# Optimization experiments

Measured on AMD Instinct MI355X. Metric: run time of the kernel, lower is better.

Reference implementation:

```python
import jax, jax.numpy as jnp
import numpy as np

N, E, NF, EF = 2048, 65536, 128, 64
HID, NH, HD, FF, L = 256, 8, 32, 1024, 4
OUT, MAXN = 1280, 4096


def setup_inputs() -> dict:
    key = jax.random.key(0)
    ks = iter(jax.random.split(key, 64))
    def rn(shape, s=0.02):
        return jax.random.normal(next(ks), shape, jnp.float32) * s
    inp = dict(
        node_features=jax.random.normal(next(ks), (N, NF), jnp.float32),
        edge_features=jax.random.normal(next(ks), (E, EF), jnp.float32),
        edge_index=jax.random.randint(next(ks), (2, E), 0, N),
        W_node=rn((NF, HID)), b_node=jnp.zeros((HID,)),
        W_edge=rn((EF, HID)), b_edge=jnp.zeros((HID,)),
        pos_emb=rn((MAXN, HID), 1.0),
        Wq=rn((L, HID, HID)), bq=jnp.zeros((L, HID)),
        Wk=rn((L, HID, HID)), bk=jnp.zeros((L, HID)),
        Wv=rn((L, HID, HID)), bv=jnp.zeros((L, HID)),
        Wo=rn((L, HID, HID)), bo=jnp.zeros((L, HID)),
        Wep=rn((L, HID, NH)), bep=jnp.zeros((L, NH)),
        Wf1=rn((L, HID, FF)), bf1=jnp.zeros((L, FF)),
        Wf2=rn((L, FF, HID)), bf2=jnp.zeros((L, HID)),
        g1=jnp.ones((L, HID)), be1=jnp.zeros((L, HID)),
        g2=jnp.ones((L, HID)), be2=jnp.zeros((L, HID)),
        g_ln=jnp.ones((HID,)), b_ln=jnp.zeros((HID,)),
        Wp1=rn((HID, HID)), bp1=jnp.zeros((HID,)),
        Wp2=rn((HID, 1)), bp2=jnp.zeros((1,)),
        Wo1=rn((3 * HID, 2 * HID)), bo1=jnp.zeros((2 * HID,)),
        Wo2=rn((2 * HID, OUT)), bo2=jnp.zeros((OUT,)),
    )
    return inp


def _ln(x, g, b, eps=1e-5):
    m = x.mean(-1, keepdims=True)
    v = ((x - m) ** 2).mean(-1, keepdims=True)
    return (x - m) * jax.lax.rsqrt(v + eps) * g + b


def reference(node_features, edge_features, edge_index, W_node, b_node, W_edge,
              b_edge, pos_emb, Wq, bq, Wk, bk, Wv, bv, Wo, bo, Wep, bep,
              Wf1, bf1, Wf2, bf2, g1, be1, g2, be2, g_ln, b_ln,
              Wp1, bp1, Wp2, bp2, Wo1, bo1, Wo2, bo2):
    n = node_features.shape[0]
    src, dst = edge_index[0], edge_index[1]
    scale = float(np.sqrt(HD))
    # node encoding + learned positional embedding (n <= max_nodes path)
    x = node_features @ W_node + b_node + pos_emb[:n]
    edge_attr = edge_features @ W_edge + b_edge  # [E, HID]
    # symmetric adjacency mask with self-loops
    adj = jnp.zeros((n, n), bool).at[src, dst].set(True).at[dst, src].set(True)
    adj = adj.at[jnp.arange(n), jnp.arange(n)].set(True)
    for i in range(L):
        Q = (x @ Wq[i] + bq[i]).reshape(n, NH, HD)
        K = (x @ Wk[i] + bk[i]).reshape(n, NH, HD)
        V = (x @ Wv[i] + bv[i]).reshape(n, NH, HD)
        scores = jnp.einsum('nhd,mhd->nmh', Q, K) / scale  # [n, n, NH]
        ebias = edge_attr @ Wep[i] + bep[i]  # [E, NH]
        scores = scores.at[src, dst].add(ebias)  # accumulating scatter, same as per-edge loop
        scores = jnp.where(adj[:, None, :], scores.transpose(0, 2, 1), -jnp.inf)  # [n, NH, n]
        attn = jax.nn.softmax(scores, axis=-1)
        ctx = jnp.einsum('nhm,mhd->nhd', attn, V).reshape(n, HID)
        a = ctx @ Wo[i] + bo[i]
        x = _ln(x + a, g1[i], be1[i])
        f = jax.nn.gelu(x @ Wf1[i] + bf1[i], approximate=False) @ Wf2[i] + bf2[i]
        x = _ln(x + f, g2[i], be2[i])
    x = _ln(x, g_ln, b_ln)
    # global pooling (batch=None path): mean / max / attention
    mean_p = x.mean(0, keepdims=True)
    max_p = x.max(0, keepdims=True)
    aw = jax.nn.softmax(jnp.tanh(x @ Wp1 + bp1) @ Wp2 + bp2, axis=0)  # [n, 1]
    attn_p = (x * aw).sum(0, keepdims=True)
    g = jnp.concatenate([mean_p, max_p, attn_p], axis=1)  # [1, 3*HID]
    out = jax.nn.relu(g @ Wo1 + bo1) @ Wo2 + bo2  # [1, OUT]
    return out
```

## Files before the change

kernel.cpp:

```cpp
#include <hip/hip_runtime.h>
#include <math.h>

#define NNODE 2048
#define NEDGE 65536
#define HIDN  256
#define NHEAD 8
#define HDIM  32
#define FFD   1024
#define NLAYER 4
#define OUTD  1280
#define NNZ_MAX (2*NEDGE + NNODE)

typedef __attribute__((ext_vector_type(8))) short bf16x8;
typedef __attribute__((ext_vector_type(4))) float f32x4;

__device__ __forceinline__ unsigned short f2b(float f) {
    unsigned u = __float_as_uint(f);
    unsigned r = (u + 0x7fffu + ((u >> 16) & 1u)) >> 16;
    return (unsigned short)r;
}
__device__ __forceinline__ float b2f(unsigned short u) {
    return __uint_as_float((unsigned)u << 16);
}

template<int K, int EPI, int OUT>
__global__ __launch_bounds__(256)
void mgemm(const unsigned short* __restrict__ A, const unsigned short* __restrict__ Bt,
           const float* __restrict__ bias, const float* __restrict__ extra,
           float* __restrict__ Cf, unsigned short* __restrict__ Cb,
           int M, int N, const float* __restrict__ Wp2, float* __restrict__ sred)
{
    __shared__ __align__(16) unsigned short As[64 * 40];
    __shared__ __align__(16) unsigned short Bs[64 * 40];
    int tid = threadIdx.x;
    int bm0 = blockIdx.y * 64, bn0 = blockIdx.x * 64;
    int wave = tid >> 6, lane = tid & 63;
    int wm = (wave >> 1) * 32, wn = (wave & 1) * 32;
    int srow = tid >> 2, skoff = (tid & 3) * 8;
    int lrow = lane & 15, quad = lane >> 4;
    const unsigned short* ap = A  + (size_t)(bm0 + srow) * K + skoff;
    const unsigned short* bp = Bt + (size_t)(bn0 + srow) * K + skoff;
    uint4 av = *(const uint4*)ap;
    uint4 bv = *(const uint4*)bp;
    f32x4 acc[2][2] = {};
    constexpr int NC = K / 32;
    #pragma unroll 8
    for (int c = 0; c < NC; ++c) {
        *(uint4*)(&As[srow*40 + skoff]) = av;
        *(uint4*)(&Bs[srow*40 + skoff]) = bv;
        __syncthreads();
        if (c + 1 < NC) {
            av = *(const uint4*)(ap + (c+1)*32);
            bv = *(const uint4*)(bp + (c+1)*32);
        }
        bf16x8 af[2], bfr[2];
        #pragma unroll
        for (int i = 0; i < 2; i++) af[i]  = *(const bf16x8*)(&As[(wm + i*16 + lrow)*40 + quad*8]);
        #pragma unroll
        for (int j = 0; j < 2; j++) bfr[j] = *(const bf16x8*)(&Bs[(wn + j*16 + lrow)*40 + quad*8]);
        #pragma unroll
        for (int i = 0; i < 2; i++)
            #pragma unroll
            for (int j = 0; j < 2; j++)
                acc[i][j] = __builtin_amdgcn_mfma_f32_16x16x32_bf16(af[i], bfr[j], acc[i][j], 0, 0, 0);
        __syncthreads();
    }
    if (EPI == 4) {
        #pragma unroll
        for (int i = 0; i < 2; i++) {
            #pragma unroll
            for (int r = 0; r < 4; r++) {
                int row = bm0 + wm + i*16 + quad*4 + r;
                float ps = 0.f;
                #pragma unroll
                for (int j = 0; j < 2; j++) {
                    int col = bn0 + wn + j*16 + lrow;
                    float v = tanhf(acc[i][j][r] + bias[col]);
                    ps += v * Wp2[col];
                }
                ps += __shfl_xor(ps, 1);
                ps += __shfl_xor(ps, 2);
                ps += __shfl_xor(ps, 4);
                ps += __shfl_xor(ps, 8);
                if (lrow == 0) atomicAdd(&sred[row], ps);
            }
        }
        return;
    }
    #pragma unroll
    for (int i = 0; i < 2; i++)
        #pragma unroll
        for (int j = 0; j < 2; j++) {
            int col = bn0 + wn + j*16 + lrow;
            float bvv = bias[col];
            #pragma unroll
            for (int r = 0; r < 4; r++) {
                int row = bm0 + wm + i*16 + quad*4 + r;
                float v = acc[i][j][r] + bvv;
                if (EPI == 1) v = 0.5f * v * (1.f + erff(v * 0.70710678118654752f));
                else if (EPI == 2) v = tanhf(v);
                else if (EPI == 3) v += extra[(size_t)row*N + col];
                if (OUT == 0 || OUT == 2) Cf[(size_t)row*N + col] = v;
                if (OUT == 1 || OUT == 2) Cb[(size_t)row*N + col] = f2b(v);
            }
        }
}

__global__ __launch_bounds__(256)
void transpose_all(const float* __restrict__ Wq, const float* __restrict__ Wk,
                   const float* __restrict__ Wv, const float* __restrict__ Wo,
                   const float* __restrict__ Wf1, const float* __restrict__ Wf2,
                   const float* __restrict__ W_node, const float* __restrict__ Wp1,
                   unsigned short* __restrict__ WqkvT, unsigned short* __restrict__ WoT,
                   unsigned short* __restrict__ Wf1T, unsigned short* __restrict__ Wf2T,
                   unsigned short* __restrict__ WnT, unsigned short* __restrict__ Wp1T)
{
    __shared__ unsigned short tile[32][33];
    int bid = blockIdx.x;
    const float* s; unsigned short* d; int K, N, n0, k0;
    if (bid < 1024) {
        int mat = bid >> 6, rem = bid & 63;
        int m4 = mat & 3, l = mat >> 2;
        s = (m4 == 0 ? Wq : m4 == 1 ? Wk : m4 == 2 ? Wv : Wo) + (size_t)l * 65536;
        d = (m4 < 3) ? WqkvT + (size_t)l*196608 + (size_t)m4*65536
                     : WoT + (size_t)l*65536;
        K = 256; N = 256; n0 = (rem & 7) * 32; k0 = (rem >> 3) * 32;
    } else if (bid < 2048) {
        int idx = bid - 1024; int l = idx >> 8, rem = idx & 255;
        s = Wf1 + (size_t)l*262144; d = Wf1T + (size_t)l*262144;
        K = 256; N = 1024; n0 = (rem & 31) * 32; k0 = (rem >> 5) * 32;
    } else if (bid < 3072) {
        int idx = bid - 2048; int l = idx >> 8, rem = idx & 255;
        s = Wf2 + (size_t)l*262144; d = Wf2T + (size_t)l*262144;
        K = 1024; N = 256; n0 = (rem & 7) * 32; k0 = (rem >> 3) * 32;
    } else if (bid < 3104) {
        int rem = bid - 3072;
        s = W_node; d = WnT;
        K = 128; N = 256; n0 = (rem & 7) * 32; k0 = (rem >> 3) * 32;
    } else {
        int rem = bid - 3104;
        s = Wp1; d = Wp1T;
        K = 256; N = 256; n0 = (rem & 7) * 32; k0 = (rem >> 3) * 32;
    }
    int tx = threadIdx.x & 31, ty = threadIdx.x >> 5;
    #pragma unroll
    for (int i = 0; i < 4; i++)
        tile[ty + i*8][tx] = f2b(s[(size_t)(k0 + ty + i*8) * N + n0 + tx]);
    __syncthreads();
    #pragma unroll
    for (int i = 0; i < 4; i++)
        d[(size_t)(n0 + ty + i*8) * K + k0 + tx] = tile[tx][ty + i*8];
}

__global__ void misc_prep(const float* __restrict__ nf, unsigned short* __restrict__ nf_b,
                          const float* __restrict__ bq, const float* __restrict__ bk,
                          const float* __restrict__ bv, float* __restrict__ bqkv)
{
    int t = blockIdx.x * 256 + threadIdx.x;
    if (t < NNODE*128) {
        nf_b[t] = f2b(nf[t]);
    } else {
        int u = t - NNODE*128;
        if (u < NLAYER*768) {
            int l = u / 768, j = u % 768;
            float v = (j < 256) ? bq[l*256 + j] : (j < 512 ? bk[l*256 + j - 256] : bv[l*256 + j - 512]);
            bqkv[u] = v;
        }
    }
}

__global__ void adj_build(const int* __restrict__ src, const int* __restrict__ dst,
                          unsigned* __restrict__ adjbits)
{
    int t = blockIdx.x * blockDim.x + threadIdx.x;
    if (t < NEDGE) {
        int s = src[t], d = dst[t];
        atomicOr(&adjbits[(size_t)s*64 + (d >> 5)], 1u << (d & 31));
        atomicOr(&adjbits[(size_t)d*64 + (s >> 5)], 1u << (s & 31));
    }
    if (t < NNODE)
        atomicOr(&adjbits[(size_t)t*64 + (t >> 5)], 1u << (t & 31));
}

__global__ void row_rank(const unsigned* __restrict__ adjbits,
                         unsigned* __restrict__ rowcum, int* __restrict__ deg)
{
    int i = blockIdx.x * blockDim.x + threadIdx.x;
    if (i >= NNODE) return;
    unsigned c = 0;
    for (int w = 0; w < 64; w++) {
        rowcum[i*64 + w] = c;
        c += __popc(adjbits[i*64 + w]);
    }
    deg[i] = (int)c;
}

__global__ __launch_bounds__(256)
void scan_kernel(const int* __restrict__ deg, int* __restrict__ rowoff)
{
    __shared__ int part[256];
    int tid = threadIdx.x;
// ... 113 lines not shown
            float p  = __expf(s - mn);
            ushort4 vu = *(const ushort4*)(QKVb + (size_t)j*768 + 512 + off);
            acc.x = acc.x*sc + p*b2f(vu.x);
            acc.y = acc.y*sc + p*b2f(vu.y);
            acc.z = acc.z*sc + p*b2f(vu.z);
            acc.w = acc.w*sc + p*b2f(vu.w);
            l = l*sc + p;
            m = mn;
        }
    }
    if ((lane & 7) == 0) { mS[w][h] = m; lS[w][h] = l; }
    *(float4*)&accS[w][off] = acc;
    __syncthreads();
    if (w == 0) {
        float m0 = mS[0][h], m1 = mS[1][h], m2 = mS[2][h], m3 = mS[3][h];
        float mx = fmaxf(fmaxf(m0, m1), fmaxf(m2, m3));
        float e0 = (m0 == -INFINITY) ? 0.f : __expf(m0 - mx);
        float e1 = (m1 == -INFINITY) ? 0.f : __expf(m1 - mx);
        float e2 = (m2 == -INFINITY) ? 0.f : __expf(m2 - mx);
        float e3 = (m3 == -INFINITY) ? 0.f : __expf(m3 - mx);
        float ls = lS[0][h]*e0 + lS[1][h]*e1 + lS[2][h]*e2 + lS[3][h]*e3;
        float4 a0 = *(float4*)&accS[0][off];
        float4 a1 = *(float4*)&accS[1][off];
        float4 a2 = *(float4*)&accS[2][off];
        float4 a3 = *(float4*)&accS[3][off];
        float inv = 1.f / ls;
        ushort4 o;
        o.x = f2b((a0.x*e0 + a1.x*e1 + a2.x*e2 + a3.x*e3) * inv);
        o.y = f2b((a0.y*e0 + a1.y*e1 + a2.y*e2 + a3.y*e3) * inv);
        o.z = f2b((a0.z*e0 + a1.z*e1 + a2.z*e2 + a3.z*e3) * inv);
        o.w = f2b((a0.w*e0 + a1.w*e1 + a2.w*e2 + a3.w*e3) * inv);
        *(ushort4*)(ctxb + (size_t)i*HIDN + off) = o;
    }
}

template<bool RES>
__global__ __launch_bounds__(256)
void ln_kernel(float* __restrict__ x, const float* __restrict__ r,
               const float* __restrict__ g, const float* __restrict__ b,
               unsigned short* __restrict__ xb)
{
    __shared__ float lds[4];
    int row = blockIdx.x, c = threadIdx.x;
    float v = x[(size_t)row*HIDN + c];
    if (RES) v += r[(size_t)row*HIDN + c];
    float s = v;
    for (int mm = 1; mm < 64; mm <<= 1) s += __shfl_xor(s, mm);
    if ((c & 63) == 0) lds[c >> 6] = s;
    __syncthreads();
    float mean = (lds[0] + lds[1] + lds[2] + lds[3]) * (1.f / HIDN);
    __syncthreads();
    float dv = v - mean;
    float qq = dv * dv;
    for (int mm = 1; mm < 64; mm <<= 1) qq += __shfl_xor(qq, mm);
    if ((c & 63) == 0) lds[c >> 6] = qq;
    __syncthreads();
    float var = (lds[0] + lds[1] + lds[2] + lds[3]) * (1.f / HIDN);
    float rs = rsqrtf(var + 1e-5f);
    float o = dv * rs * g[c] + b[c];
    x[(size_t)row*HIDN + c] = o;
    xb[(size_t)row*HIDN + c] = f2b(o);
}

__global__ __launch_bounds__(256)
void pool_part(const float* __restrict__ x, const float* __restrict__ sred,
               float* __restrict__ partial)
{
    __shared__ float red[4];
    __shared__ float aw[128];
    int b = blockIdx.x, tid = threadIdx.x;
    float mxs = -INFINITY;
    for (int r = tid; r < NNODE; r += 256) mxs = fmaxf(mxs, sred[r]);
    for (int mm = 1; mm < 64; mm <<= 1) mxs = fmaxf(mxs, __shfl_xor(mxs, mm));
    if ((tid & 63) == 0) red[tid >> 6] = mxs;
    __syncthreads();
    mxs = fmaxf(fmaxf(red[0], red[1]), fmaxf(red[2], red[3]));
    __syncthreads();
    float ss = 0.f;
    for (int r = tid; r < NNODE; r += 256) ss += __expf(sred[r] - mxs);
    for (int mm = 1; mm < 64; mm <<= 1) ss += __shfl_xor(ss, mm);
    if ((tid & 63) == 0) red[tid >> 6] = ss;
    __syncthreads();
    ss = red[0] + red[1] + red[2] + red[3];
    float inv = 1.f / ss;
    int r0 = b * 128;
    if (tid < 128) aw[tid] = __expf(sred[r0 + tid] - mxs) * inv;
    __syncthreads();
    float sm = 0.f, mx = -INFINITY, ap = 0.f;
    for (int r = 0; r < 128; r++) {
        float v = x[(size_t)(r0 + r)*HIDN + tid];
        sm += v;
        mx = fmaxf(mx, v);
        ap += v * aw[r];
    }
// ... 75 lines not shown
    const float* bv = (const float*)d_in[13];
    const float* Wo = (const float*)d_in[14];
    const float* bo = (const float*)d_in[15];
    const float* Wep = (const float*)d_in[16];
    const float* bep = (const float*)d_in[17];
    const float* Wf1 = (const float*)d_in[18];
    const float* bf1 = (const float*)d_in[19];
    const float* Wf2 = (const float*)d_in[20];
    const float* bf2 = (const float*)d_in[21];
    const float* g1  = (const float*)d_in[22];
    const float* be1 = (const float*)d_in[23];
    const float* g2  = (const float*)d_in[24];
    const float* be2 = (const float*)d_in[25];
    const float* g_ln = (const float*)d_in[26];
    const float* b_ln = (const float*)d_in[27];
    const float* Wp1 = (const float*)d_in[28];
    const float* bp1 = (const float*)d_in[29];
    const float* Wp2 = (const float*)d_in[30];
    const float* bp2 = (const float*)d_in[31];
    const float* Wo1 = (const float*)d_in[32];
    const float* bo1 = (const float*)d_in[33];
    const float* Wo2 = (const float*)d_in[34];
    const float* bo2 = (const float*)d_in[35];
    (void)bp2;
    const int* src = edge_index;
    const int* dst = edge_index + NEDGE;

    char* w = (char*)d_ws;
    auto carve = [&](size_t nbytes) {
        void* p = (void*)w;
        w += (nbytes + 255) & ~(size_t)255;
        return p;
    };
    float* x        = (float*)carve((size_t)NNODE*HIDN*4);
    unsigned short* xb = (unsigned short*)carve((size_t)NNODE*HIDN*2);
    unsigned short* bufQKVb = (unsigned short*)carve((size_t)NNODE*768*2);
    float* bufO     = (float*)carve((size_t)NNODE*HIDN*4);
    unsigned short* bufAb = (unsigned short*)carve((size_t)NNODE*HIDN*2);
    unsigned short* bufFb = (unsigned short*)carve((size_t)NNODE*FFD*2);
    float* Wcomb    = (float*)carve(64*32*4);
    float* bcomb    = (float*)carve(32*4);
    unsigned* adjbits = (unsigned*)carve((size_t)NNODE*64*4);
    float* bias_csr = (float*)carve((size_t)NNZ_MAX*32*4);
    float* sbuf  = (float*)carve(NNODE*4);
    unsigned* rowcum  = (unsigned*)carve((size_t)NNODE*64*4);
    int* deg    = (int*)carve(NNODE*4);
    int* rowoff = (int*)carve((NNODE+1)*4);
    int* colsb  = (int*)carve((size_t)NNZ_MAX*4);
    float* gbuf  = (float*)carve(3*HIDN*4);
    float* partial = (float*)carve(16*768*4);
    float* h1buf = (float*)carve(512*4);
    unsigned short* nf_b  = (unsigned short*)carve((size_t)NNODE*128*2);
    unsigned short* WnT   = (unsigned short*)carve((size_t)HIDN*128*2);
    unsigned short* WqkvT = (unsigned short*)carve((size_t)NLAYER*768*HIDN*2);
    float*          bqkv  = (float*)carve((size_t)NLAYER*768*4);
    unsigned short* WoT   = (unsigned short*)carve((size_t)NLAYER*HIDN*HIDN*2);
    unsigned short* Wf1T  = (unsigned short*)carve((size_t)NLAYER*FFD*HIDN*2);
    unsigned short* Wf2T  = (unsigned short*)carve((size_t)NLAYER*HIDN*FFD*2);
    unsigned short* Wp1T  = (unsigned short*)carve((size_t)HIDN*HIDN*2);

    hipMemsetAsync(adjbits, 0,
                   (size_t)NNODE*64*4 + (size_t)NNZ_MAX*32*4 + (size_t)NNODE*4, stream);
    adj_build<<<(NEDGE+255)/256, 256, 0, stream>>>(src, dst, adjbits);
    row_rank<<<NNODE/256, 256, 0, stream>>>(adjbits, rowcum, deg);
    scan_kernel<<<1, 256, 0, stream>>>(deg, rowoff);
    fill_cols<<<(NNODE*64)/256, 256, 0, stream>>>(adjbits, rowoff, rowcum, colsb);
    wcomb_kernel<<<(64*32+32+255)/256, 256, 0, stream>>>(W_edge, b_edge, Wep, bep, Wcomb, bcomb);
    edge_bias_scatter<<<(NEDGE*32)/256, 256, 0, stream>>>(
        edge_features, Wcomb, bcomb, src, dst, adjbits, rowcum, rowoff, bias_csr);

    misc_prep<<<(NNODE*128 + NLAYER*768 + 255)/256, 256, 0, stream>>>(
        node_features, nf_b, bq, bk, bv, bqkv);
    transpose_all<<<3168, 256, 0, stream>>>(Wq, Wk, Wv, Wo, Wf1, Wf2, W_node, Wp1,
                                            WqkvT, WoT, Wf1T, Wf2T, WnT, Wp1T);

    mgemm<128,3,2><<<dim3(HIDN/64, NNODE/64), 256, 0, stream>>>(
        nf_b, WnT, b_node, pos_emb, x, xb, NNODE, HIDN, nullptr, nullptr);

    for (int l = 0; l < NLAYER; l++) {
        mgemm<256,0,1><<<dim3(768/64, NNODE/64), 256, 0, stream>>>(
            xb, WqkvT + (size_t)l*768*HIDN, bqkv + l*768, nullptr, nullptr, bufQKVb, NNODE, 768, nullptr, nullptr);
        attn_kernel<<<NNODE, 256, 0, stream>>>(bufQKVb, rowoff, colsb, bias_csr, bufAb, l);
        mgemm<256,0,0><<<dim3(HIDN/64, NNODE/64), 256, 0, stream>>>(
            bufAb, WoT + (size_t)l*HIDN*HIDN, bo + l*HIDN, nullptr, bufO, nullptr, NNODE, HIDN, nullptr, nullptr);
        ln_kernel<true><<<NNODE, 256, 0, stream>>>(x, bufO, g1 + l*HIDN, be1 + l*HIDN, xb);
        mgemm<256,1,1><<<dim3(FFD/64, NNODE/64), 256, 0, stream>>>(
            xb, Wf1T + (size_t)l*FFD*HIDN, bf1 + l*FFD, nullptr, nullptr, bufFb, NNODE, FFD, nullptr, nullptr);
        mgemm<1024,0,0><<<dim3(HIDN/64, NNODE/64), 256, 0, stream>>>(
            bufFb, Wf2T + (size_t)l*HIDN*FFD, bf2 + l*HIDN, nullptr, bufO, nullptr, NNODE, HIDN, nullptr, nullptr);
        ln_kernel<true><<<NNODE, 256, 0, stream>>>(x, bufO, g2 + l*HIDN, be2 + l*HIDN, xb);
    }

    ln_kernel<false><<<NNODE, 256, 0, stream>>>(x, nullptr, g_ln, b_ln, xb);
    mgemm<256,4,0><<<dim3(HIDN/64, NNODE/64), 256, 0, stream>>>(
        xb, Wp1T, bp1, nullptr, nullptr, nullptr, NNODE, HIDN, Wp2, sbuf);
    pool_part<<<16, 256, 0, stream>>>(x, sbuf, partial);
    pool_fin<<<1, 256, 0, stream>>>(partial, gbuf);
    head1<<<8, 256, 0, stream>>>(gbuf, Wo1, bo1, h1buf);
    head2<<<OUTD/64, 256, 0, stream>>>(h1buf, Wo2, bo2, (float*)d_out);
}
```

Baseline: 462.4 us.

## Fuse output and FFN2 GEMMs with residual LayerNorm; merge prep kernels

```diff
diff --git a/kernel.cpp b/kernel.cpp
--- a/kernel.cpp
+++ b/kernel.cpp
@@ -98,12 +98,154 @@
                 int row = bm0 + wm + i*16 + quad*4 + r;
                 float v = acc[i][j][r] + bvv;
                 if (EPI == 1) v = 0.5f * v * (1.f + erff(v * 0.70710678118654752f));
-                else if (EPI == 2) v = tanhf(v);
                 else if (EPI == 3) v += extra[(size_t)row*N + col];
                 if (OUT == 0 || OUT == 2) Cf[(size_t)row*N + col] = v;
                 if (OUT == 1 || OUT == 2) Cb[(size_t)row*N + col] = f2b(v);
             }
         }
+}
+
+template<int K, bool DOUBLE>
+__global__ __launch_bounds__(256)
+void mgemm_ln(const unsigned short* __restrict__ A, const unsigned short* __restrict__ Bt,
+              const float* __restrict__ bias, const float* __restrict__ res,
+              const float* __restrict__ ga, const float* __restrict__ ba,
+              const float* __restrict__ gb, const float* __restrict__ bb,
+              float* __restrict__ X, unsigned short* __restrict__ Xb)
+{
+    __shared__ __align__(16) unsigned short As[16 * 40];
+    __shared__ __align__(16) unsigned short Bs[256 * 40];
+    __shared__ float rsum[4][16], rsq[4][16], rsum2[4][16], rsq2[4][16];
+    int tid = threadIdx.x;
+    int bm0 = blockIdx.x * 16;
+    int w = tid >> 6, lane = tid & 63;
+    int lrow = lane & 15, quad = lane >> 4;
+    int arow = tid >> 2, akoff = (tid & 3) * 8;
+    const unsigned short* ap = A + (size_t)(bm0 + arow) * K + akoff;
+    const unsigned short* bp = Bt + (size_t)tid * K;
+    uint4 av, bv0, bv1, bv2, bv3;
+    if (tid < 64) av = *(const uint4*)ap;
+    bv0 = *(const uint4*)(bp + 0);
+    bv1 = *(const uint4*)(bp + 8);
+    bv2 = *(const uint4*)(bp + 16);
+    bv3 = *(const uint4*)(bp + 24);
+    f32x4 acc[4] = {};
+    constexpr int NC = K / 32;
+    #pragma unroll 8
+    for (int c = 0; c < NC; ++c) {
+        if (tid < 64) *(uint4*)(&As[arow*40 + akoff]) = av;
+        *(uint4*)(&Bs[tid*40 + 0])  = bv0;
+        *(uint4*)(&Bs[tid*40 + 8])  = bv1;
+        *(uint4*)(&Bs[tid*40 + 16]) = bv2;
+        *(uint4*)(&Bs[tid*40 + 24]) = bv3;
+        __syncthreads();
+        if (c + 1 < NC) {
+            if (tid < 64) av = *(const uint4*)(ap + (c+1)*32);
+            bv0 = *(const uint4*)(bp + (c+1)*32 + 0);
+            bv1 = *(const uint4*)(bp + (c+1)*32 + 8);
+            bv2 = *(const uint4*)(bp + (c+1)*32 + 16);
+            bv3 = *(const uint4*)(bp + (c+1)*32 + 24);
+        }
+        bf16x8 af = *(const bf16x8*)(&As[lrow*40 + quad*8]);
+        #pragma unroll
+        for (int j = 0; j < 4; j++) {
+            bf16x8 bf = *(const bf16x8*)(&Bs[(w*64 + j*16 + lrow)*40 + quad*8]);
+            acc[j] = __builtin_amdgcn_mfma_f32_16x16x32_bf16(af, bf, acc[j], 0, 0, 0);
+        }
+        __syncthreads();
+    }
+    float v[4][4];
+    #pragma unroll
+    for (int j = 0; j < 4; j++) {
+        int col = w*64 + j*16 + lrow;
+        float bvv = bias[col];
+        #pragma unroll
+        for (int r = 0; r < 4; r++) {
+            int row = bm0 + quad*4 + r;
+            v[j][r] = acc[j][r] + bvv + res[(size_t)row*HIDN + col];
+        }
+    }
+    float mean[4], rsv[4];
+    #pragma unroll
+    for (int r = 0; r < 4; r++) {
+        float s = v[0][r] + v[1][r] + v[2][r] + v[3][r];
+        s += __shfl_xor(s, 1); s += __shfl_xor(s, 2);
+        s += __shfl_xor(s, 4); s += __shfl_xor(s, 8);
+        if (lrow == 0) rsum[w][quad*4 + r] = s;
+    }
+    __syncthreads();
+    #pragma unroll
+    for (int r = 0; r < 4; r++) {
+        int rr = quad*4 + r;
+        mean[r] = (rsum[0][rr] + rsum[1][rr] + rsum[2][rr] + rsum[3][rr]) * (1.f/HIDN);
+        float q = 0.f;
+        #pragma unroll
+        for (int j = 0; j < 4; j++) { float d = v[j][r] - mean[r]; q += d*d; }
+        q += __shfl_xor(q, 1); q += __shfl_xor(q, 2);
+        q += __shfl_xor(q, 4); q += __shfl_xor(q, 8);
+        if (lrow == 0) rsq[w][rr] = q;
+    }
+    __syncthreads();
+    #pragma unroll
+    for (int r = 0; r < 4; r++) {
+        int rr = quad*4 + r;
+        float var = (rsq[0][rr] + rsq[1][rr] + rsq[2][rr] + rsq[3][rr]) * (1.f/HIDN);
+        rsv[r] = rsqrtf(var + 1e-5f);
+    }
+    #pragma unroll
+    for (int j = 0; j < 4; j++) {
+        int col = w*64 + j*16 + lrow;
+        float gv = ga[col], bvv = ba[col];
+        #pragma unroll
+        for (int r = 0; r < 4; r++)
+            v[j][r] = (v[j][r] - mean[r]) * rsv[r] * gv + bvv;
+    }
+    if (DOUBLE) {
+        #pragma unroll
+        for (int r = 0; r < 4; r++) {
+            float s = v[0][r] + v[1][r] + v[2][r] + v[3][r];
+            s += __shfl_xor(s, 1); s += __shfl_xor(s, 2);
+            s += __shfl_xor(s, 4); s += __shfl_xor(s, 8);
+            if (lrow == 0) rsum2[w][quad*4 + r] = s;
+        }
+        __syncthreads();
+        #pragma unroll
+        for (int r = 0; r < 4; r++) {
+            int rr = quad*4 + r;
+            mean[r] = (rsum2[0][rr] + rsum2[1][rr] + rsum2[2][rr] + rsum2[3][rr]) * (1.f/HIDN);
+            float q = 0.f;
+            #pragma unroll
+            for (int j = 0; j < 4; j++) { float d = v[j][r] - mean[r]; q += d*d; }
+            q += __shfl_xor(q, 1); q += __shfl_xor(q, 2);
+            q += __shfl_xor(q, 4); q += __shfl_xor(q, 8);
+            if (lrow == 0) rsq2[w][rr] = q;
+        }
+        __syncthreads();
+        #pragma unroll
+        for (int r = 0; r < 4; r++) {
+            int rr = quad*4 + r;
+            float var = (rsq2[0][rr] + rsq2[1][rr] + rsq2[2][rr] + rsq2[3][rr]) * (1.f/HIDN);
+            rsv[r] = rsqrtf(var + 1e-5f);
+        }
+        #pragma unroll
+        for (int j = 0; j < 4; j++) {
+            int col = w*64 + j*16 + lrow;
+            float gv = gb[col], bvv = bb[col];
+            #pragma unroll
+            for (int r = 0; r < 4; r++)
+                v[j][r] = (v[j][r] - mean[r]) * rsv[r] * gv + bvv;
+        }
+    }
+    #pragma unroll
+    for (int j = 0; j < 4; j++) {
+        int col = w*64 + j*16 + lrow;
+        #pragma unroll
+        for (int r = 0; r < 4; r++) {
+            int row = bm0 + quad*4 + r;
+            X[(size_t)row*HIDN + col] = v[j][r];
+            Xb[(size_t)row*HIDN + col] = f2b(v[j][r]);
+        }
+    }
 }
 
 __global__ __launch_bounds__(256)
@@ -113,10 +255,27 @@
                    const float* __restrict__ W_node, const float* __restrict__ Wp1,
                    unsigned short* __restrict__ WqkvT, unsigned short* __restrict__ WoT,
                    unsigned short* __restrict__ Wf1T, unsigned short* __restrict__ Wf2T,
-                   unsigned short* __restrict__ WnT, unsigned short* __restrict__ Wp1T)
+                   unsigned short* __restrict__ WnT, unsigned short* __restrict__ Wp1T,
+                   const float* __restrict__ nf, unsigned short* __restrict__ nf_b,
+                   const float* __restrict__ bq, const float* __restrict__ bk,
+                   const float* __restrict__ bv, float* __restrict__ bqkv)
 {
     __shared__ unsigned short tile[32][33];
     int bid = blockIdx.x;
+    if (bid >= 3168) {
+        int t = (bid - 3168) * 256 + threadIdx.x;
+        if (t < NNODE*128) {
+            nf_b[t] = f2b(nf[t]);
+        } else {
+            int u = t - NNODE*128;
+            if (u < NLAYER*768) {
+                int l = u / 768, j = u % 768;
+                float vv = (j < 256) ? bq[l*256 + j] : (j < 512 ? bk[l*256 + j - 256] : bv[l*256 + j - 512]);
+                bqkv[u] = vv;
+            }
+        }
+        return;
+    }
     const float* s; unsigned short* d; int K, N, n0, k0;
     if (bid < 1024) {
         int mat = bid >> 6, rem = bid & 63;
@@ -150,23 +309,6 @@
     #pragma unroll
     for (int i = 0; i < 4; i++)
         d[(size_t)(n0 + ty + i*8) * K + k0 + tx] = tile[tx][ty + i*8];
-}
-
-__global__ void misc_prep(const float* __restrict__ nf, unsigned short* __restrict__ nf_b,
-                          const float* __restrict__ bq, const float* __restrict__ bk,
-                          const float* __restrict__ bv, float* __restrict__ bqkv)
-{
-    int t = blockIdx.x * 256 + threadIdx.x;
-    if (t < NNODE*128) {
-        nf_b[t] = f2b(nf[t]);
-    } else {
-        int u = t - NNODE*128;
-        if (u < NLAYER*768) {
-            int l = u / 768, j = u % 768;
-            float v = (j < 256) ? bq[l*256 + j] : (j < 512 ? bk[l*256 + j - 256] : bv[l*256 + j - 512]);
-            bqkv[u] = v;
-        }
-    }
 }
 
 __global__ void adj_build(const int* __restrict__ src, const int* __restrict__ dst,
@@ -346,34 +488,6 @@
         o.w = f2b((a0.w*e0 + a1.w*e1 + a2.w*e2 + a3.w*e3) * inv);
         *(ushort4*)(ctxb + (size_t)i*HIDN + off) = o;
     }
-}
-
-template<bool RES>
-__global__ __launch_bounds__(256)
-void ln_kernel(float* __restrict__ x, const float* __restrict__ r,
-               const float* __restrict__ g, const float* __restrict__ b,
-               unsigned short* __restrict__ xb)
-{
-    __shared__ float lds[4];
-    int row = blockIdx.x, c = threadIdx.x;
-    float v = x[(size_t)row*HIDN + c];
-    if (RES) v += r[(size_t)row*HIDN + c];
-    float s = v;
-    for (int mm = 1; mm < 64; mm <<= 1) s += __shfl_xor(s, mm);
-    if ((c & 63) == 0) lds[c >> 6] = s;
-    __syncthreads();
-    float mean = (lds[0] + lds[1] + lds[2] + lds[3]) * (1.f / HIDN);
-    __syncthreads();
-    float dv = v - mean;
-    float qq = dv * dv;
-    for (int mm = 1; mm < 64; mm <<= 1) qq += __shfl_xor(qq, mm);
-    if ((c & 63) == 0) lds[c >> 6] = qq;
-    __syncthreads();
-    float var = (lds[0] + lds[1] + lds[2] + lds[3]) * (1.f / HIDN);
-    float rs = rsqrtf(var + 1e-5f);
-    float o = dv * rs * g[c] + b[c];
-    x[(size_t)row*HIDN + c] = o;
-    xb[(size_t)row*HIDN + c] = f2b(o);
 }
 
 __global__ __launch_bounds__(256)
@@ -518,7 +632,6 @@
     float* x        = (float*)carve((size_t)NNODE*HIDN*4);
     unsigned short* xb = (unsigned short*)carve((size_t)NNODE*HIDN*2);
     unsigned short* bufQKVb = (unsigned short*)carve((size_t)NNODE*768*2);
-    float* bufO     = (float*)carve((size_t)NNODE*HIDN*4);
     unsigned short* bufAb = (unsigned short*)carve((size_t)NNODE*HIDN*2);
     unsigned short* bufFb = (unsigned short*)carve((size_t)NNODE*FFD*2);
     float* Wcomb    = (float*)carve(64*32*4);
@@ -552,10 +665,10 @@
     edge_bias_scatter<<<(NEDGE*32)/256, 256, 0, stream>>>(
         edge_features, Wcomb, bcomb, src, dst, adjbits, rowcum, rowoff, bias_csr);
 
-    misc_prep<<<(NNODE*128 + NLAYER*768 + 255)/256, 256, 0, stream>>>(
+    transpose_all<<<3168 + 1024 + 12, 256, 0, stream>>>(
+        Wq, Wk, Wv, Wo, Wf1, Wf2, W_node, Wp1,
+        WqkvT, WoT, Wf1T, Wf2T, WnT, Wp1T,
         node_features, nf_b, bq, bk, bv, bqkv);
-    transpose_all<<<3168, 256, 0, stream>>>(Wq, Wk, Wv, Wo, Wf1, Wf2, W_node, Wp1,
-                                            WqkvT, WoT, Wf1T, Wf2T, WnT, Wp1T);
 
     mgemm<128,3,2><<<dim3(HIDN/64, NNODE/64), 256, 0, stream>>>(
         nf_b, WnT, b_node, pos_emb, x, xb, NNODE, HIDN, nullptr, nullptr);
@@ -564,17 +677,21 @@
         mgemm<256,0,1><<<dim3(768/64, NNODE/64), 256, 0, stream>>>(
             xb, WqkvT + (size_t)l*768*HIDN, bqkv + l*768, nullptr, nullptr, bufQKVb, NNODE, 768, nullptr, nullptr);
         attn_kernel<<<NNODE, 256, 0, stream>>>(bufQKVb, rowoff, colsb, bias_csr, bufAb, l);
-        mgemm<256,0,0><<<dim3(HIDN/64, NNODE/64), 256, 0, stream>>>(
-            bufAb, WoT + (size_t)l*HIDN*HIDN, bo + l*HIDN, nullptr, bufO, nullptr, NNODE, HIDN, nullptr, nullptr);
-        ln_kernel<true><<<NNODE, 256, 0, stream>>>(x, bufO, g1 + l*HIDN, be1 + l*HIDN, xb);
+        mgemm_ln<256,false><<<NNODE/16, 256, 0, stream>>>(
+            bufAb, WoT + (size_t)l*HIDN*HIDN, bo + l*HIDN, x,
+            g1 + l*HIDN, be1 + l*HIDN, nullptr, nullptr, x, xb);
         mgemm<256,1,1><<<dim3(FFD/64, NNODE/64), 256, 0, stream>>>(
             xb, Wf1T + (size_t)l*FFD*HIDN, bf1 + l*FFD, nullptr, nullptr, bufFb, NNODE, FFD, nullptr, nullptr);
-        mgemm<1024,0,0><<<dim3(HIDN/64, NNODE/64), 256, 0, stream>>>(
-            bufFb, Wf2T + (size_t)l*HIDN*FFD, bf2 + l*HIDN, nullptr, bufO, nullptr, NNODE, HIDN, nullptr, nullptr);
-        ln_kernel<true><<<NNODE, 256, 0, stream>>>(x, bufO, g2 + l*HIDN, be2 + l*HIDN, xb);
-    }
-
-    ln_kernel<false><<<NNODE, 256, 0, stream>>>(x, nullptr, g_ln, b_ln, xb);
+        if (l < NLAYER - 1)
+            mgemm_ln<1024,false><<<NNODE/16, 256, 0, stream>>>(
+                bufFb, Wf2T + (size_t)l*HIDN*FFD, bf2 + l*HIDN, x,
+                g2 + l*HIDN, be2 + l*HIDN, nullptr, nullptr, x, xb);
+        else
+            mgemm_ln<1024,true><<<NNODE/16, 256, 0, stream>>>(
+                bufFb, Wf2T + (size_t)l*HIDN*FFD, bf2 + l*HIDN, x,
+                g2 + l*HIDN, be2 + l*HIDN, g_ln, b_ln, x, xb);
+    }
+
     mgemm<256,4,0><<<dim3(HIDN/64, NNODE/64), 256, 0, stream>>>(
         xb, Wp1T, bp1, nullptr, nullptr, nullptr, NNODE, HIDN, Wp2, sbuf);
     pool_part<<<16, 256, 0, stream>>>(x, sbuf, partial);
```

Measured after the change: 515.1 us. +11.4%, slower.

## Fuse residual LayerNorm into following GEMM prologue and merge prep kernels

Applied to the files above, without the earlier changes.

```diff
diff --git a/kernel.cpp b/kernel.cpp
--- a/kernel.cpp
+++ b/kernel.cpp
@@ -98,10 +98,152 @@
                 int row = bm0 + wm + i*16 + quad*4 + r;
                 float v = acc[i][j][r] + bvv;
                 if (EPI == 1) v = 0.5f * v * (1.f + erff(v * 0.70710678118654752f));
-                else if (EPI == 2) v = tanhf(v);
                 else if (EPI == 3) v += extra[(size_t)row*N + col];
                 if (OUT == 0 || OUT == 2) Cf[(size_t)row*N + col] = v;
                 if (OUT == 1 || OUT == 2) Cb[(size_t)row*N + col] = f2b(v);
+            }
+        }
+}
+
+template<int EPI, int OUT, bool DBL>
+__global__ __launch_bounds__(256)
+void mgemm_pro(const float* __restrict__ pre, const float* __restrict__ res,
+               const unsigned short* __restrict__ Bt, const float* __restrict__ bias,
+               const float* __restrict__ ga, const float* __restrict__ ba,
+               const float* __restrict__ gb, const float* __restrict__ bb,
+               float* __restrict__ Cf, unsigned short* __restrict__ Cb,
+               float* __restrict__ xout,
+               int M, int N, const float* __restrict__ Wp2, float* __restrict__ sred)
+{
+    __shared__ __align__(16) unsigned short As[64 * 264];
+    __shared__ __align__(16) unsigned short Bs[64 * 40];
+    int tid = threadIdx.x;
+    int bm0 = blockIdx.y * 64, bn0 = blockIdx.x * 64;
+    int wave = tid >> 6, lane = tid & 63;
+    int wm = (wave >> 1) * 32, wn = (wave & 1) * 32;
+    int lrow = lane & 15, quad = lane >> 4;
+    int prow = tid >> 2, pcb = (tid & 3) * 4;
+    const float* pp = pre + (size_t)(bm0 + prow) * HIDN + pcb;
+    const float* rp = res + (size_t)(bm0 + prow) * HIDN + pcb;
+    float4 v[16];
+    float sum = 0.f;
+    #pragma unroll
+    for (int i = 0; i < 16; i++) {
+        float4 a = *(const float4*)(pp + i*16);
+        float4 b = *(const float4*)(rp + i*16);
+        a.x += b.x; a.y += b.y; a.z += b.z; a.w += b.w;
+        v[i] = a;
+        sum += a.x + a.y + a.z + a.w;
+    }
+    sum += __shfl_xor(sum, 1); sum += __shfl_xor(sum, 2);
+    float mean = sum * (1.f/256.f);
+    float sq = 0.f;
+    #pragma unroll
+    for (int i = 0; i < 16; i++) {
+        float dx = v[i].x-mean, dy = v[i].y-mean, dz = v[i].z-mean, dw = v[i].w-mean;
+        sq += dx*dx + dy*dy + dz*dz + dw*dw;
+    }
+    sq += __shfl_xor(sq, 1); sq += __shfl_xor(sq, 2);
+    float rs = rsqrtf(sq * (1.f/256.f) + 1e-5f);
+    #pragma unroll
+    for (int i = 0; i < 16; i++) {
+        float4 g4 = *(const float4*)(ga + pcb + i*16);
+        float4 b4 = *(const float4*)(ba + pcb + i*16);
+        v[i].x = (v[i].x - mean) * rs * g4.x + b4.x;
+        v[i].y = (v[i].y - mean) * rs * g4.y + b4.y;
+        v[i].z = (v[i].z - mean) * rs * g4.z + b4.z;
+        v[i].w = (v[i].w - mean) * rs * g4.w + b4.w;
+    }
+    if (DBL) {
+        sum = 0.f;
+        #pragma unroll
+        for (int i = 0; i < 16; i++) sum += v[i].x + v[i].y + v[i].z + v[i].w;
+        sum += __shfl_xor(sum, 1); sum += __shfl_xor(sum, 2);
+        mean = sum * (1.f/256.f);
+        sq = 0.f;
+        #pragma unroll
+        for (int i = 0; i < 16; i++) {
+            float dx = v[i].x-mean, dy = v[i].y-mean, dz = v[i].z-mean, dw = v[i].w-mean;
+            sq += dx*dx + dy*dy + dz*dz + dw*dw;
+        }
+        sq += __shfl_xor(sq, 1); sq += __shfl_xor(sq, 2);
+        rs = rsqrtf(sq * (1.f/256.f) + 1e-5f);
+        #pragma unroll
+        for (int i = 0; i < 16; i++) {
+            float4 g4 = *(const float4*)(gb + pcb + i*16);
+            float4 b4 = *(const float4*)(bb + pcb + i*16);
+            v[i].x = (v[i].x - mean) * rs * g4.x + b4.x;
+            v[i].y = (v[i].y - mean) * rs * g4.y + b4.y;
+            v[i].z = (v[i].z - mean) * rs * g4.z + b4.z;
+            v[i].w = (v[i].w - mean) * rs * g4.w + b4.w;
+        }
+    }
+    #pragma unroll
+    for (int i = 0; i < 16; i++) {
+        ushort4 us = { f2b(v[i].x), f2b(v[i].y), f2b(v[i].z), f2b(v[i].w) };
+        *(ushort4*)(&As[prow*264 + pcb + i*16]) = us;
+    }
+    if (bn0 == 0) {
+        float* xp = xout + (size_t)(bm0 + prow) * HIDN + pcb;
+        #pragma unroll
+        for (int i = 0; i < 16; i++) *(float4*)(xp + i*16) = v[i];
+    }
+    int srow = tid >> 2, skoff = (tid & 3) * 8;
+    const unsigned short* bp = Bt + (size_t)(bn0 + srow) * HIDN + skoff;
+    uint4 bv = *(const uint4*)bp;
+    f32x4 acc[2][2] = {};
+    #pragma unroll
+    for (int c = 0; c < 8; ++c) {
+        *(uint4*)(&Bs[srow*40 + skoff]) = bv;
+        __syncthreads();
+        if (c + 1 < 8) bv = *(const uint4*)(bp + (c+1)*32);
+        bf16x8 af[2], bfr[2];
+        #pragma unroll
+        for (int i = 0; i < 2; i++) af[i]  = *(const bf16x8*)(&As[(wm + i*16 + lrow)*264 + c*32 + quad*8]);
+        #pragma unroll
+        for (int j = 0; j < 2; j++) bfr[j] = *(const bf16x8*)(&Bs[(wn + j*16 + lrow)*40 + quad*8]);
+        #pragma unroll
+        for (int i = 0; i < 2; i++)
+            #pragma unroll
+            for (int j = 0; j < 2; j++)
+                acc[i][j] = __builtin_amdgcn_mfma_f32_16x16x32_bf16(af[i], bfr[j], acc[i][j], 0, 0, 0);
+        __syncthreads();
+    }
+    if (EPI == 4) {
+        #pragma unroll
+        for (int i = 0; i < 2; i++) {
+            #pragma unroll
+            for (int r = 0; r < 4; r++) {
+                int row = bm0 + wm + i*16 + quad*4 + r;
+                float ps = 0.f;
+                #pragma unroll
+                for (int j = 0; j < 2; j++) {
+                    int col = bn0 + wn + j*16 + lrow;
+                    float vv = tanhf(acc[i][j][r] + bias[col]);
+                    ps += vv * Wp2[col];
+                }
+                ps += __shfl_xor(ps, 1);
+                ps += __shfl_xor(ps, 2);
+                ps += __shfl_xor(ps, 4);
+                ps += __shfl_xor(ps, 8);
+                if (lrow == 0) atomicAdd(&sred[row], ps);
+            }
+        }
+        return;
+    }
+    #pragma unroll
+    for (int i = 0; i < 2; i++)
+        #pragma unroll
+        for (int j = 0; j < 2; j++) {
+            int col = bn0 + wn + j*16 + lrow;
+            float bvv = bias[col];
+            #pragma unroll
+            for (int r = 0; r < 4; r++) {
+                int row = bm0 + wm + i*16 + quad*4 + r;
+                float vv = acc[i][j][r] + bvv;
+                if (EPI == 1) vv = 0.5f * vv * (1.f + erff(vv * 0.70710678118654752f));
+                if (OUT == 0) Cf[(size_t)row*N + col] = vv;
+                else          Cb[(size_t)row*N + col] = f2b(vv);
             }
         }
 }
@@ -113,10 +255,27 @@
                    const float* __restrict__ W_node, const float* __restrict__ Wp1,
                    unsigned short* __restrict__ WqkvT, unsigned short* __restrict__ WoT,
                    unsigned short* __restrict__ Wf1T, unsigned short* __restrict__ Wf2T,
-                   unsigned short* __restrict__ WnT, unsigned short* __restrict__ Wp1T)
+                   unsigned short* __restrict__ WnT, unsigned short* __restrict__ Wp1T,
+                   const float* __restrict__ nf, unsigned short* __restrict__ nf_b,
+                   const float* __restrict__ bq, const float* __restrict__ bk,
+                   const float* __restrict__ bv, float* __restrict__ bqkv)
 {
     __shared__ unsigned short tile[32][33];
     int bid = blockIdx.x;
+    if (bid >= 3168) {
+        int t = (bid - 3168) * 256 + threadIdx.x;
+        if (t < NNODE*128) {
+            nf_b[t] = f2b(nf[t]);
+        } else {
+            int u = t - NNODE*128;
+            if (u < NLAYER*768) {
+                int l = u / 768, j = u % 768;
+                float vv = (j < 256) ? bq[l*256 + j] : (j < 512 ? bk[l*256 + j - 256] : bv[l*256 + j - 512]);
+                bqkv[u] = vv;
+            }
+        }
+        return;
+    }
     const float* s; unsigned short* d; int K, N, n0, k0;
     if (bid < 1024) {
         int mat = bid >> 6, rem = bid & 63;
@@ -150,23 +309,6 @@
     #pragma unroll
     for (int i = 0; i < 4; i++)
         d[(size_t)(n0 + ty + i*8) * K + k0 + tx] = tile[tx][ty + i*8];
-}
-
-__global__ void misc_prep(const float* __restrict__ nf, unsigned short* __restrict__ nf_b,
-                          const float* __restrict__ bq, const float* __restrict__ bk,
-                          const float* __restrict__ bv, float* __restrict__ bqkv)
-{
-    int t = blockIdx.x * 256 + threadIdx.x;
-    if (t < NNODE*128) {
-        nf_b[t] = f2b(nf[t]);
-    } else {
-        int u = t - NNODE*128;
-        if (u < NLAYER*768) {
-            int l = u / 768, j = u % 768;
-            float v = (j < 256) ? bq[l*256 + j] : (j < 512 ? bk[l*256 + j - 256] : bv[l*256 + j - 512]);
-            bqkv[u] = v;
-        }
-    }
 }
 
 __global__ void adj_build(const int* __restrict__ src, const int* __restrict__ dst,
@@ -346,34 +488,6 @@
         o.w = f2b((a0.w*e0 + a1.w*e1 + a2.w*e2 + a3.w*e3) * inv);
         *(ushort4*)(ctxb + (size_t)i*HIDN + off) = o;
     }
-}
-
-template<bool RES>
-__global__ __launch_bounds__(256)
-void ln_kernel(float* __restrict__ x, const float* __restrict__ r,
-               const float* __restrict__ g, const float* __restrict__ b,
-               unsigned short* __restrict__ xb)
-{
-    __shared__ float lds[4];
-    int row = blockIdx.x, c = threadIdx.x;
-    float v = x[(size_t)row*HIDN + c];
-    if (RES) v += r[(size_t)row*HIDN + c];
-    float s = v;
-    for (int mm = 1; mm < 64; mm <<= 1) s += __shfl_xor(s, mm);
-    if ((c & 63) == 0) lds[c >> 6] = s;
-    __syncthreads();
-    float mean = (lds[0] + lds[1] + lds[2] + lds[3]) * (1.f / HIDN);
-    __syncthreads();
-    float dv = v - mean;
-    float qq = dv * dv;
-    for (int mm = 1; mm < 64; mm <<= 1) qq += __shfl_xor(qq, mm);
-    if ((c & 63) == 0) lds[c >> 6] = qq;
-    __syncthreads();
-    float var = (lds[0] + lds[1] + lds[2] + lds[3]) * (1.f / HIDN);
-    float rs = rsqrtf(var + 1e-5f);
-    float o = dv * rs * g[c] + b[c];
-    x[(size_t)row*HIDN + c] = o;
-    xb[(size_t)row*HIDN + c] = f2b(o);
 }
 
 __global__ __launch_bounds__(256)
@@ -515,7 +629,8 @@
         w += (nbytes + 255) & ~(size_t)255;
         return p;
     };
-    float* x        = (float*)carve((size_t)NNODE*HIDN*4);
+    float* xA       = (float*)carve((size_t)NNODE*HIDN*4);
+    float* xB       = (float*)carve((size_t)NNODE*HIDN*4);
     unsigned short* xb = (unsigned short*)carve((size_t)NNODE*HIDN*2);
     unsigned short* bufQKVb = (unsigned short*)carve((size_t)NNODE*768*2);
     float* bufO     = (float*)carve((size_t)NNODE*HIDN*4);
@@ -552,32 +667,45 @@
     edge_bias_scatter<<<(NEDGE*32)/256, 256, 0, stream>>>(
         edge_features, Wcomb, bcomb, src, dst, adjbits, rowcum, rowoff, bias_csr);
 
-    misc_prep<<<(NNODE*128 + NLAYER*768 + 255)/256, 256, 0, stream>>>(
+    transpose_all<<<3168 + 1024 + 12, 256, 0, stream>>>(
+        Wq, Wk, Wv, Wo, Wf1, Wf2, W_node, Wp1,
+        WqkvT, WoT, Wf1T, Wf2T, WnT, Wp1T,
         node_features, nf_b, bq, bk, bv, bqkv);
-    transpose_all<<<3168, 256, 0, stream>>>(Wq, Wk, Wv, Wo, Wf1, Wf2, W_node, Wp1,
-                                            WqkvT, WoT, Wf1T, Wf2T, WnT, Wp1T);
 
     mgemm<128,3,2><<<dim3(HIDN/64, NNODE/64), 256, 0, stream>>>(
-        nf_b, WnT, b_node, pos_emb, x, xb, NNODE, HIDN, nullptr, nullptr);
+        nf_b, WnT, b_node, pos_emb, xA, xb, NNODE, HIDN, nullptr, nullptr);
+
+    float* xcur = xA;
+    float* xnxt = xB;
 
     for (int l = 0; l < NLAYER; l++) {
-        mgemm<256,0,1><<<dim3(768/64, NNODE/64), 256, 0, stream>>>(
-            xb, WqkvT + (size_t)l*768*HIDN, bqkv + l*768, nullptr, nullptr, bufQKVb, NNODE, 768, nullptr, nullptr);
+        if (l == 0) {
+            mgemm<256,0,1><<<dim3(768/64, NNODE/64), 256, 0, stream>>>(
+                xb, WqkvT, bqkv, nullptr, nullptr, bufQKVb, NNODE, 768, nullptr, nullptr);
+        } else {
+            mgemm_pro<0,1,false><<<dim3(768/64, NNODE/64), 256, 0, stream>>>(
+                bufO, xcur, WqkvT + (size_t)l*768*HIDN, bqkv + l*768,
+                g2 + (l-1)*HIDN, be2 + (l-1)*HIDN, nullptr, nullptr,
+                nullptr, bufQKVb, xnxt, NNODE, 768, nullptr, nullptr);
+            { float* t = xcur; xcur = xnxt; xnxt = t; }
+        }
         attn_kernel<<<NNODE, 256, 0, stream>>>(bufQKVb, rowoff, colsb, bias_csr, bufAb, l);
         mgemm<256,0,0><<<dim3(HIDN/64, NNODE/64), 256, 0, stream>>>(
             bufAb, WoT + (size_t)l*HIDN*HIDN, bo + l*HIDN, nullptr, bufO, nullptr, NNODE, HIDN, nullptr, nullptr);
-        ln_kernel<true><<<NNODE, 256, 0, stream>>>(x, bufO, g1 + l*HIDN, be1 + l*HIDN, xb);
-        mgemm<256,1,1><<<dim3(FFD/64, NNODE/64), 256, 0, stream>>>(
-            xb, Wf1T + (size_t)l*FFD*HIDN, bf1 + l*FFD, nullptr, nullptr, bufFb, NNODE, FFD, nullptr, nullptr);
+        mgemm_pro<1,1,false><<<dim3(FFD/64, NNODE/64), 256, 0, stream>>>(
+            bufO, xcur, Wf1T + (size_t)l*FFD*HIDN, bf1 + l*FFD,
+            g1 + l*HIDN, be1 + l*HIDN, nullptr, nullptr,
+            nullptr, bufFb, xnxt, NNODE, FFD, nullptr, nullptr);
+        { float* t = xcur; xcur = xnxt; xnxt = t; }
         mgemm<1024,0,0><<<dim3(HIDN/64, NNODE/64), 256, 0, stream>>>(
             bufFb, Wf2T + (size_t)l*HIDN*FFD, bf2 + l*HIDN, nullptr, bufO, nullptr, NNODE, HIDN, nullptr, nullptr);
-        ln_kernel<true><<<NNODE, 256, 0, stream>>>(x, bufO, g2 + l*HIDN, be2 + l*HIDN, xb);
-    }
-
-    ln_kernel<false><<<NNODE, 256, 0, stream>>>(x, nullptr, g_ln, b_ln, xb);
-    mgemm<256,4,0><<<dim3(HIDN/64, NNODE/64), 256, 0, stream>>>(
-        xb, Wp1T, bp1, nullptr, nullptr, nullptr, NNODE, HIDN, Wp2, sbuf);
-    pool_part<<<16, 256, 0, stream>>>(x, sbuf, partial);
+    }
+
+    mgemm_pro<4,0,true><<<dim3(HIDN/64, NNODE/64), 256, 0, stream>>>(
+        bufO, xcur, Wp1T, bp1,
+        g2 + 3*HIDN, be2 + 3*HIDN, g_ln, b_ln,
+        nullptr, nullptr, xnxt, NNODE, HIDN, Wp2, sbuf);
+    pool_part<<<16, 256, 0, stream>>>(xnxt, sbuf, partial);
     pool_fin<<<1, 256, 0, stream>>>(partial, gbuf);
     head1<<<8, 256, 0, stream>>>(gbuf, Wo1, bo1, h1buf);
     head2<<<OUTD/64, 256, 0, stream>>>(h1buf, Wo2, bo2, (float*)d_out);
```

Result: slower. 483.7 us (+4.6%).

## Shrink GEMM M-tile to 32 with double-buffered LDS and merge prep kernels

Applied to the files above, without the earlier changes.

```diff
diff --git a/kernel.cpp b/kernel.cpp
--- a/kernel.cpp
+++ b/kernel.cpp
@@ -30,80 +30,78 @@
            float* __restrict__ Cf, unsigned short* __restrict__ Cb,
            int M, int N, const float* __restrict__ Wp2, float* __restrict__ sred)
 {
-    __shared__ __align__(16) unsigned short As[64 * 40];
-    __shared__ __align__(16) unsigned short Bs[64 * 40];
+    __shared__ __align__(16) unsigned short As[2][32 * 40];
+    __shared__ __align__(16) unsigned short Bs[2][64 * 40];
     int tid = threadIdx.x;
-    int bm0 = blockIdx.y * 64, bn0 = blockIdx.x * 64;
+    int bm0 = blockIdx.y * 32, bn0 = blockIdx.x * 64;
     int wave = tid >> 6, lane = tid & 63;
-    int wm = (wave >> 1) * 32, wn = (wave & 1) * 32;
-    int srow = tid >> 2, skoff = (tid & 3) * 8;
+    int wm = (wave >> 1) * 16;
+    int wn = (wave & 1) * 32;
     int lrow = lane & 15, quad = lane >> 4;
-    const unsigned short* ap = A  + (size_t)(bm0 + srow) * K + skoff;
-    const unsigned short* bp = Bt + (size_t)(bn0 + srow) * K + skoff;
-    uint4 av = *(const uint4*)ap;
-    uint4 bv = *(const uint4*)bp;
-    f32x4 acc[2][2] = {};
+    int brow = tid >> 2, koff = (tid & 3) * 8;
+    int arow = (tid & 127) >> 2;
+    bool doA = tid < 128;
+    const unsigned short* ap = A  + (size_t)(bm0 + arow) * K + koff;
+    const unsigned short* bp = Bt + (size_t)(bn0 + brow) * K + koff;
+    uint4 av, bv;
+    if (doA) av = *(const uint4*)ap;
+    bv = *(const uint4*)bp;
     constexpr int NC = K / 32;
+    if (doA) *(uint4*)(&As[0][arow*40 + koff]) = av;
+    *(uint4*)(&Bs[0][brow*40 + koff]) = bv;
+    __syncthreads();
+    f32x4 acc[2] = {};
     #pragma unroll 8
     for (int c = 0; c < NC; ++c) {
-        *(uint4*)(&As[srow*40 + skoff]) = av;
-        *(uint4*)(&Bs[srow*40 + skoff]) = bv;
-        __syncthreads();
+        int cur = c & 1;
         if (c + 1 < NC) {
-            av = *(const uint4*)(ap + (c+1)*32);
+            if (doA) av = *(const uint4*)(ap + (c+1)*32);
             bv = *(const uint4*)(bp + (c+1)*32);
         }
-        bf16x8 af[2], bfr[2];
-        #pragma unroll
-        for (int i = 0; i < 2; i++) af[i]  = *(const bf16x8*)(&As[(wm + i*16 + lrow)*40 + quad*8]);
-        #pragma unroll
-        for (int j = 0; j < 2; j++) bfr[j] = *(const bf16x8*)(&Bs[(wn + j*16 + lrow)*40 + quad*8]);
-        #pragma unroll
-        for (int i = 0; i < 2; i++)
-            #pragma unroll
-            for (int j = 0; j < 2; j++)
-                acc[i][j] = __builtin_amdgcn_mfma_f32_16x16x32_bf16(af[i], bfr[j], acc[i][j], 0, 0, 0);
+        bf16x8 af = *(const bf16x8*)(&As[cur][(wm + lrow)*40 + quad*8]);
+        bf16x8 b0 = *(const bf16x8*)(&Bs[cur][(wn + lrow)*40 + quad*8]);
+        bf16x8 b1 = *(const bf16x8*)(&Bs[cur][(wn + 16 + lrow)*40 + quad*8]);
+        acc[0] = __builtin_amdgcn_mfma_f32_16x16x32_bf16(af, b0, acc[0], 0, 0, 0);
+        acc[1] = __builtin_amdgcn_mfma_f32_16x16x32_bf16(af, b1, acc[1], 0, 0, 0);
+        if (c + 1 < NC) {
+            if (doA) *(uint4*)(&As[cur^1][arow*40 + koff]) = av;
+            *(uint4*)(&Bs[cur^1][brow*40 + koff]) = bv;
+        }
         __syncthreads();
     }
     if (EPI == 4) {
         #pragma unroll
-        for (int i = 0; i < 2; i++) {
+        for (int r = 0; r < 4; r++) {
+            int row = bm0 + wm + quad*4 + r;
+            float ps = 0.f;
             #pragma unroll
-            for (int r = 0; r < 4; r++) {
-                int row = bm0 + wm + i*16 + quad*4 + r;
-                float ps = 0.f;
-                #pragma unroll
-                for (int j = 0; j < 2; j++) {
-                    int col = bn0 + wn + j*16 + lrow;
-                    float v = tanhf(acc[i][j][r] + bias[col]);
-                    ps += v * Wp2[col];
-                }
-                ps += __shfl_xor(ps, 1);
-                ps += __shfl_xor(ps, 2);
-                ps += __shfl_xor(ps, 4);
-                ps += __shfl_xor(ps, 8);
-                if (lrow == 0) atomicAdd(&sred[row], ps);
+            for (int j = 0; j < 2; j++) {
+                int col = bn0 + wn + j*16 + lrow;
+                float v = tanhf(acc[j][r] + bias[col]);
+                ps += v * Wp2[col];
             }
+            ps += __shfl_xor(ps, 1);
+            ps += __shfl_xor(ps, 2);
+            ps += __shfl_xor(ps, 4);
+            ps += __shfl_xor(ps, 8);
+            if (lrow == 0) atomicAdd(&sred[row], ps);
         }
         return;
     }
     #pragma unroll
-    for (int i = 0; i < 2; i++)
+    for (int j = 0; j < 2; j++) {
+        int col = bn0 + wn + j*16 + lrow;
+        float bvv = bias[col];
         #pragma unroll
-        for (int j = 0; j < 2; j++) {
-            int col = bn0 + wn + j*16 + lrow;
-            float bvv = bias[col];
-            #pragma unroll
-            for (int r = 0; r < 4; r++) {
-                int row = bm0 + wm + i*16 + quad*4 + r;
-                float v = acc[i][j][r] + bvv;
-                if (EPI == 1) v = 0.5f * v * (1.f + erff(v * 0.70710678118654752f));
-                else if (EPI == 2) v = tanhf(v);
-                else if (EPI == 3) v += extra[(size_t)row*N + col];
-                if (OUT == 0 || OUT == 2) Cf[(size_t)row*N + col] = v;
-                if (OUT == 1 || OUT == 2) Cb[(size_t)row*N + col] = f2b(v);
-            }
+        for (int r = 0; r < 4; r++) {
+            int row = bm0 + wm + quad*4 + r;
+            float v = acc[j][r] + bvv;
+            if (EPI == 1) v = 0.5f * v * (1.f + erff(v * 0.70710678118654752f));
+            else if (EPI == 3) v += extra[(size_t)row*N + col];
+            if (OUT == 0 || OUT == 2) Cf[(size_t)row*N + col] = v;
+            if (OUT == 1 || OUT == 2) Cb[(size_t)row*N + col] = f2b(v);
         }
+    }
 }
 
 __global__ __launch_bounds__(256)
@@ -113,10 +111,27 @@
                    const float* __restrict__ W_node, const float* __restrict__ Wp1,
                    unsigned short* __restrict__ WqkvT, unsigned short* __restrict__ WoT,
                    unsigned short* __restrict__ Wf1T, unsigned short* __restrict__ Wf2T,
-                   unsigned short* __restrict__ WnT, unsigned short* __restrict__ Wp1T)
+                   unsigned short* __restrict__ WnT, unsigned short* __restrict__ Wp1T,
+                   const float* __restrict__ nf, unsigned short* __restrict__ nf_b,
+                   const float* __restrict__ bq, const float* __restrict__ bk,
+                   const float* __restrict__ bv, float* __restrict__ bqkv)
 {
     __shared__ unsigned short tile[32][33];
     int bid = blockIdx.x;
+    if (bid >= 3168) {
+        int t = (bid - 3168) * 256 + threadIdx.x;
+        if (t < NNODE*128) {
+            nf_b[t] = f2b(nf[t]);
+        } else {
+            int u = t - NNODE*128;
+            if (u < NLAYER*768) {
+                int l = u / 768, j = u % 768;
+                float vv = (j < 256) ? bq[l*256 + j] : (j < 512 ? bk[l*256 + j - 256] : bv[l*256 + j - 512]);
+                bqkv[u] = vv;
+            }
+        }
+        return;
+    }
     const float* s; unsigned short* d; int K, N, n0, k0;
     if (bid < 1024) {
         int mat = bid >> 6, rem = bid & 63;
@@ -150,23 +165,6 @@
     #pragma unroll
     for (int i = 0; i < 4; i++)
         d[(size_t)(n0 + ty + i*8) * K + k0 + tx] = tile[tx][ty + i*8];
-}
-
-__global__ void misc_prep(const float* __restrict__ nf, unsigned short* __restrict__ nf_b,
-                          const float* __restrict__ bq, const float* __restrict__ bk,
-                          const float* __restrict__ bv, float* __restrict__ bqkv)
-{
-    int t = blockIdx.x * 256 + threadIdx.x;
-    if (t < NNODE*128) {
-        nf_b[t] = f2b(nf[t]);
-    } else {
-        int u = t - NNODE*128;
-        if (u < NLAYER*768) {
-            int l = u / 768, j = u % 768;
-            float v = (j < 256) ? bq[l*256 + j] : (j < 512 ? bk[l*256 + j - 256] : bv[l*256 + j - 512]);
-            bqkv[u] = v;
-        }
-    }
 }
 
 __global__ void adj_build(const int* __restrict__ src, const int* __restrict__ dst,
@@ -552,30 +550,30 @@
     edge_bias_scatter<<<(NEDGE*32)/256, 256, 0, stream>>>(
         edge_features, Wcomb, bcomb, src, dst, adjbits, rowcum, rowoff, bias_csr);
 
-    misc_prep<<<(NNODE*128 + NLAYER*768 + 255)/256, 256, 0, stream>>>(
+    transpose_all<<<3168 + 1024 + 12, 256, 0, stream>>>(
+        Wq, Wk, Wv, Wo, Wf1, Wf2, W_node, Wp1,
+        WqkvT, WoT, Wf1T, Wf2T, WnT, Wp1T,
         node_features, nf_b, bq, bk, bv, bqkv);
-    transpose_all<<<3168, 256, 0, stream>>>(Wq, Wk, Wv, Wo, Wf1, Wf2, W_node, Wp1,
-                                            WqkvT, WoT, Wf1T, Wf2T, WnT, Wp1T);
-
-    mgemm<128,3,2><<<dim3(HIDN/64, NNODE/64), 256, 0, stream>>>(
+
+    mgemm<128,3,2><<<dim3(HIDN/64, NNODE/32), 256, 0, stream>>>(
         nf_b, WnT, b_node, pos_emb, x, xb, NNODE, HIDN, nullptr, nullptr);
 
     for (int l = 0; l < NLAYER; l++) {
-        mgemm<256,0,1><<<dim3(768/64, NNODE/64), 256, 0, stream>>>(
+        mgemm<256,0,1><<<dim3(768/64, NNODE/32), 256, 0, stream>>>(
             xb, WqkvT + (size_t)l*768*HIDN, bqkv + l*768, nullptr, nullptr, bufQKVb, NNODE, 768, nullptr, nullptr);
         attn_kernel<<<NNODE, 256, 0, stream>>>(bufQKVb, rowoff, colsb, bias_csr, bufAb, l);
-        mgemm<256,0,0><<<dim3(HIDN/64, NNODE/64), 256, 0, stream>>>(
+        mgemm<256,0,0><<<dim3(HIDN/64, NNODE/32), 256, 0, stream>>>(
             bufAb, WoT + (size_t)l*HIDN*HIDN, bo + l*HIDN, nullptr, bufO, nullptr, NNODE, HIDN, nullptr, nullptr);
         ln_kernel<true><<<NNODE, 256, 0, stream>>>(x, bufO, g1 + l*HIDN, be1 + l*HIDN, xb);
-        mgemm<256,1,1><<<dim3(FFD/64, NNODE/64), 256, 0, stream>>>(
+        mgemm<256,1,1><<<dim3(FFD/64, NNODE/32), 256, 0, stream>>>(
             xb, Wf1T + (size_t)l*FFD*HIDN, bf1 + l*FFD, nullptr, nullptr, bufFb, NNODE, FFD, nullptr, nullptr);
-        mgemm<1024,0,0><<<dim3(HIDN/64, NNODE/64), 256, 0, stream>>>(
+        mgemm<1024,0,0><<<dim3(HIDN/64, NNODE/32), 256, 0, stream>>>(
             bufFb, Wf2T + (size_t)l*HIDN*FFD, bf2 + l*HIDN, nullptr, bufO, nullptr, NNODE, HIDN, nullptr, nullptr);
         ln_kernel<true><<<NNODE, 256, 0, stream>>>(x, bufO, g2 + l*HIDN, be2 + l*HIDN, xb);
     }
 
     ln_kernel<false><<<NNODE, 256, 0, stream>>>(x, nullptr, g_ln, b_ln, xb);
-    mgemm<256,4,0><<<dim3(HIDN/64, NNODE/64), 256, 0, stream>>>(
+    mgemm<256,4,0><<<dim3(HIDN/64, NNODE/32), 256, 0, stream>>>(
         xb, Wp1T, bp1, nullptr, nullptr, nullptr, NNODE, HIDN, Wp2, sbuf);
     pool_part<<<16, 256, 0, stream>>>(x, sbuf, partial);
     pool_fin<<<1, 256, 0, stream>>>(partial, gbuf);
```

New measurement: 453.3 us. About the same (-2.0%).
